# Kernel tuning notes

Hardware: AMD Instinct MI355X
Metric: run time of the kernel (lower is better)

## Reference

```python
import jax, jax.numpy as jnp
import numpy as np

B, S, D = 2, 2048, 2048
NH, NKV, HD = 16, 4, 128
REP = NH // NKV
EPS = 1e-6
ROPE_THETA = 1e6


def setup_inputs() -> dict:
    key = jax.random.key(0)
    ks = jax.random.split(key, 6)
    x = jax.random.normal(ks[0], (B, S, D), jnp.float32)
    # real rotary embeddings: [S, HD]
    inv_freq = 1.0 / (ROPE_THETA ** (np.arange(0, HD, 2, dtype=np.float64) / HD))
    freqs = np.outer(np.arange(S, dtype=np.float64), inv_freq)
    emb = np.concatenate([freqs, freqs], axis=-1)
    cos = jnp.asarray(np.cos(emb), jnp.float32)
    sin = jnp.asarray(np.sin(emb), jnp.float32)
    scale = 1.0 / np.sqrt(D)
    Wq = jax.random.normal(ks[1], (D, NH * HD), jnp.float32) * scale   # [in, out]
    Wk = jax.random.normal(ks[2], (D, NKV * HD), jnp.float32) * scale
    Wv = jax.random.normal(ks[3], (D, NKV * HD), jnp.float32) * scale
    Wo = jax.random.normal(ks[4], (NH * HD, D), jnp.float32) * (1.0 / np.sqrt(NH * HD))
    q_norm_w = jnp.ones((HD,), jnp.float32)
    k_norm_w = jnp.ones((HD,), jnp.float32)
    return dict(x=x, cos=cos, sin=sin, Wq=Wq, Wk=Wk, Wv=Wv, Wo=Wo,
                q_norm_w=q_norm_w, k_norm_w=k_norm_w)


def _rms_norm(h, w):
    var = jnp.mean(h * h, axis=-1, keepdims=True)
    return w * (h * jax.lax.rsqrt(var + EPS))


def _rotate_half(h):
    h1, h2 = jnp.split(h, 2, axis=-1)
    return jnp.concatenate([-h2, h1], axis=-1)


def reference(x, cos, sin, Wq, Wk, Wv, Wo, q_norm_w, k_norm_w):
    b, s, _ = x.shape
    q = (x @ Wq).reshape(b, s, NH, HD)
    k = (x @ Wk).reshape(b, s, NKV, HD)
    v = (x @ Wv).reshape(b, s, NKV, HD)
    # per-head QK RMSNorm
    q = _rms_norm(q, q_norm_w)
    k = _rms_norm(k, k_norm_w)
    # RoPE: cos/sin [S,HD] -> broadcast over batch and heads
    c = cos[None, :, None, :]
    s_ = sin[None, :, None, :]
    q = q * c + _rotate_half(q) * s_
    k = k * c + _rotate_half(k) * s_
    # GQA: group q heads per kv head instead of materializing repeat_kv
    qg = q.reshape(b, s, NKV, REP, HD)
    scores = jnp.einsum('bqgrd,bkgd->bgrqk', qg, k) / np.sqrt(HD)
    causal = jnp.tril(jnp.ones((s, s), bool))  # [q,k]
    scores = jnp.where(causal, scores, -jnp.inf)
    probs = jax.nn.softmax(scores.astype(jnp.float32), axis=-1).astype(q.dtype)
    out = jnp.einsum('bgrqk,bkgd->bqgrd', probs, v).reshape(b, s, NH * HD)
    return out @ Wo
```

## Files before the change

### kernel.cpp

```cpp
#include <hip/hip_runtime.h>
#include <hip/hip_bf16.h>
#include <math.h>

#define B_ 2
#define S_ 2048
#define D_ 2048
#define NH_ 16
#define NKV_ 4
#define HD_ 128
#define EPS_ 1e-6f
#define SCALE_ 0.08838834764831845f
#define LOG2E_ 1.4426950408889634f
#define NQKV_ 3072
#define KOFF_ 2048
#define VOFF_ 2560

typedef float f32x4 __attribute__((ext_vector_type(4)));
typedef short bf16x8 __attribute__((ext_vector_type(8)));
typedef short short4v __attribute__((ext_vector_type(4)));
typedef float float4v __attribute__((ext_vector_type(4)));
typedef unsigned uint2v __attribute__((ext_vector_type(2)));

static __device__ __forceinline__ short f2bf(float f) {
    union { float f; unsigned u; } x{f};
    unsigned r = (x.u + 0x7fff + ((x.u >> 16) & 1)) >> 16;
    return (short)r;
}
static __device__ __forceinline__ float bf2f(short s) {
    union { unsigned u; float f; } x; x.u = ((unsigned)(unsigned short)s) << 16; return x.f;
}
static __device__ __forceinline__ unsigned pack_bf2(float a, float b) {
    return __builtin_amdgcn_perm(__builtin_bit_cast(unsigned, b),
                                 __builtin_bit_cast(unsigned, a), 0x07060302u);
}

#define AS1(p) ((const __attribute__((address_space(1))) void*)(p))
#define AS3(p) ((__attribute__((address_space(3))) void*)(p))
static __device__ __forceinline__ void async16(const void* g, void* l) {
    __builtin_amdgcn_global_load_lds(AS1(g), AS3(l), 16, 0, 0);
}

__global__ __launch_bounds__(256) void cast_kernel(const float* __restrict__ in,
                                                   short* __restrict__ out) {
    size_t i = ((size_t)blockIdx.x * 256 + threadIdx.x) * 4;
    float4v v = *(const float4v*)(in + i);
    short4v o; o.x = f2bf(v.x); o.y = f2bf(v.y); o.z = f2bf(v.z); o.w = f2bf(v.w);
    *(short4v*)(out + i) = o;
}

__global__ __launch_bounds__(256) void transpose_cast_kernel(const float* __restrict__ in,
                                                             short* __restrict__ out,
                                                             int K, int N) {
    __shared__ float tile[64][65];
    const int n0 = blockIdx.x * 64, k0 = blockIdx.y * 64;
    const int tid = threadIdx.x;
    for (int r = 0; r < 16; ++r) {
        int k = r * 4 + (tid >> 6);
        int n = tid & 63;
        tile[k][n] = in[(size_t)(k0 + k) * N + n0 + n];
    }
    __syncthreads();
    for (int r = 0; r < 4; ++r) {
        int n  = r * 16 + (tid >> 4);
        int kk = (tid & 15) * 4;
        short4v o4;
        o4.x = f2bf(tile[kk + 0][n]); o4.y = f2bf(tile[kk + 1][n]);
        o4.z = f2bf(tile[kk + 2][n]); o4.w = f2bf(tile[kk + 3][n]);
        *(short4v*)&out[(size_t)(n0 + n) * K + k0 + kk] = o4;
    }
}

template<typename TC>
__global__ __launch_bounds__(256) void gemm_tt_kernel(const short* __restrict__ A,
                                                      const short* __restrict__ Bt,
                                                      TC* __restrict__ C,
                                                      int M, int N, int K) {
    __shared__ short As[128 * 32];
    __shared__ short Bs[128 * 32];

    const int tid  = threadIdx.x;
    const int bn   = blockIdx.x, bm = blockIdx.y;
    const int wave = tid >> 6, lane = tid & 63;
    const int quad = lane >> 4, l16 = lane & 15;
    const int wr = wave >> 1, wc = wave & 1;

    f32x4 acc[4][4];
    for (int i = 0; i < 4; ++i)
        for (int j = 0; j < 4; ++j) acc[i][j] = (f32x4){0.f, 0.f, 0.f, 0.f};

    const short* Abase = A  + (size_t)(bm * 128) * K;
    const short* Bbase = Bt + (size_t)(bn * 128) * K;

    int ci0 = wave * 128 + lane;
    for (int k0 = 0; k0 < K; k0 += 32) {
        __syncthreads();
        for (int t = 0; t < 2; ++t) {
            int ci = ci0 + t * 64;
            int r  = ci >> 2;
            int c  = ((ci & 3) - (r >> 1)) & 3;
            size_t goff = (size_t)r * K + k0 + c * 8;
            async16(Abase + goff, &As[ci * 8]);
            async16(Bbase + goff, &Bs[ci * 8]);
        }
        __syncthreads();

        bf16x8 af[4], bfv[4];
        for (int mt = 0; mt < 4; ++mt) {
            int r = wr * 64 + mt * 16 + l16;
            af[mt] = *(const bf16x8*)&As[r * 32 + (((quad + (r >> 1)) & 3) * 8)];
        }
        for (int nt = 0; nt < 4; ++nt) {
            int r = wc * 64 + nt * 16 + l16;
            bfv[nt] = *(const bf16x8*)&Bs[r * 32 + (((quad + (r >> 1)) & 3) * 8)];
        }
        for (int mt = 0; mt < 4; ++mt)
            for (int nt = 0; nt < 4; ++nt)
                acc[mt][nt] = __builtin_amdgcn_mfma_f32_16x16x32_bf16(
                    af[mt], bfv[nt], acc[mt][nt], 0, 0, 0);
    }

    for (int mt = 0; mt < 4; ++mt)
        for (int nt = 0; nt < 4; ++nt)
            for (int j = 0; j < 4; ++j) {
                int row = bm * 128 + wr * 64 + mt * 16 + quad * 4 + j;
                int col = bn * 128 + wc * 64 + nt * 16 + l16;
                float v = acc[mt][nt][j];
                if constexpr (__is_same(TC, short))
                    C[(size_t)row * N + col] = f2bf(v);
                else
                    C[(size_t)row * N + col] = v;
            }
}

template<int NHEADS, bool HEAD_MAJOR>
__global__ __launch_bounds__(256) void rope_rms_kernel(const short* __restrict__ qkv,
                                                       int coloff,
                                                       const float* __restrict__ cosb,
                                                       const float* __restrict__ sinb,
                                                       const float* __restrict__ w,
                                                       short* __restrict__ out,
                                                       float outscale) {
    const int r    = blockIdx.x * 4 + (threadIdx.x >> 6);
    const int lane = threadIdx.x & 63;
    const int tok  = r / NHEADS, head = r % NHEADS;
    const int spos = tok & (S_ - 1);
    const short* row = qkv + (size_t)tok * NQKV_ + coloff + head * HD_;
    float h1 = bf2f(row[lane]), h2 = bf2f(row[lane + 64]);
    float ss = h1 * h1 + h2 * h2;
    for (int off = 1; off < 64; off <<= 1) ss += __shfl_xor(ss, off);
    float rstd = rsqrtf(ss * (1.0f / HD_) + EPS_);
    float n1 = h1 * rstd * w[lane];
    float n2 = h2 * rstd * w[lane + 64];
    float c  = cosb[spos * HD_ + lane];
    float sn = sinb[spos * HD_ + lane];
    size_t o;
    if (HEAD_MAJOR) {
        int b = tok >> 11, s = tok & (S_ - 1);
        o = ((size_t)(b * NHEADS + head) * S_ + s) * HD_;
    } else {
        o = ((size_t)tok * NHEADS + head) * HD_;
    }
    out[o + lane]      = f2bf((n1 * c - n2 * sn) * outscale);
    out[o + lane + 64] = f2bf((n2 * c + n1 * sn) * outscale);
}

__global__ __launch_bounds__(256) void vtrans_kernel(const short* __restrict__ qkv,
                                                     short* __restrict__ vt) {
    __shared__ short tile[64][71];
    const int s0 = blockIdx.x * 64, d0 = blockIdx.y * 64;
    const int g = blockIdx.z & 3, b = blockIdx.z >> 2;
    const int tid = threadIdx.x;
    for (int r = 0; r < 16; ++r) {
        int s = r * 4 + (tid >> 6);
        int d = tid & 63;
        tile[s][d] = qkv[(size_t)(b * S_ + s0 + s) * NQKV_ + VOFF_ + g * HD_ + d0 + d];
    }
    __syncthreads();
    for (int r = 0; r < 16; ++r) {
        int d = r * 4 + (tid >> 6);
        int s = tid & 63;
        vt[((size_t)(b * NKV_ + g) * HD_ + d0 + d) * S_ + s0 + s] = tile[s][d];
    }
}

__global__ __launch_bounds__(256, 2) void attn_kernel(const short* __restrict__ qr,
                                                      const short* __restrict__ kg,
                                                      const short* __restrict__ vt,
                                                      short* __restrict__ aout) {
    __shared__ short Ks[2][64 * 128];
    __shared__ short Vs[2][128 * 64];

    const int lin = blockIdx.x;
    const int b  = lin & 1;
    const int g  = (lin >> 1) & 3;
    const int hq = (lin >> 3) & 3;
    const int pr = lin >> 5;
    const int h  = g * 4 + hq;

    const int wave = threadIdx.x >> 6, lane = threadIdx.x & 63;
    const int quad = lane >> 4, l16 = lane & 15;

    const short* kbase = kg + (size_t)(b * NKV_ + g) * S_ * HD_;
    const short* vbase = vt + (size_t)(b * NKV_ + g) * HD_ * S_;

    for (int pass = 0; pass < 2; ++pass) {
        const int qt    = pass ? (31 - pr) : pr;
        const int iters = qt + 1;
        const int qrow  = qt * 64 + wave * 16 + l16;

        bf16x8 qf[4];
        {
            const short* qp = qr + ((size_t)(b * S_ + qrow) * NH_ + h) * HD_;
            for (int ks = 0; ks < 4; ++ks)
                qf[ks] = *(const bf16x8*)(qp + ks * 32 + quad * 8);
        }

        f32x4 o[8];
        for (int i = 0; i < 8; ++i) o[i] = (f32x4){0.f, 0.f, 0.f, 0.f};
        float m_i = -INFINITY, l_i = 0.f;

        auto stage = [&](int kt, int bsel) {
            const short* kt_base = kbase + (size_t)kt * 64 * HD_;
            const short* vt_base = vbase + kt * 64;
            for (int t = 0; t < 4; ++t) {
                int ci  = (wave * 4 + t) * 64 + lane;
                int key = ci >> 4;
                int c   = (ci & 15) ^ ((key ^ (key >> 2)) & 15);
                async16(kt_base + key * HD_ + c * 8, &Ks[bsel][ci * 8]);
            }
            for (int t = 0; t < 4; ++t) {
                int ci = (wave * 4 + t) * 64 + lane;
                int d  = ci >> 3;
                int c  = (ci & 7) ^ (d & 7);
                async16(vt_base + (size_t)d * S_ + c * 8, &Vs[bsel][ci * 8]);
            }
        };

        stage(0, 0);
        int buf = 0;
        for (int kt = 0; kt < iters; ++kt) {
            __syncthreads();
            if (kt + 1 < iters) stage(kt + 1, buf ^ 1);

            f32x4 acc[4];
            for (int t = 0; t < 4; ++t) acc[t] = (f32x4){0.f, 0.f, 0.f, 0.f};
            for (int t = 0; t < 4; ++t) {
                int lk = ((t >> 1) << 5) + ((l16 >> 2) << 3) + ((t & 1) << 2) + (l16 & 3);
                const short* kp = &Ks[buf][lk * 128];
                int pm = (lk ^ (lk >> 2)) & 15;
                for (int ks = 0; ks < 4; ++ks) {
                    bf16x8 kf = *(const bf16x8*)(kp + (((ks * 4 + quad) ^ pm) * 8));
                    acc[t] = __builtin_amdgcn_mfma_f32_16x16x32_bf16(kf, qf[ks], acc[t], 0, 0, 0);
                }
            }
            const int key_base = kt * 64;
            if (key_base + 63 > qt * 64 + wave * 16) {
                for (int t = 0; t < 4; ++t)
                    for (int j = 0; j < 4; ++j) {
                        int kl = key_base + ((t >> 1) << 5) + (quad << 3) + ((t & 1) << 2) + j;
                        if (kl > qrow) acc[t][j] = -INFINITY;
                    }
            }
            float mx = m_i;
            for (int t = 0; t < 4; ++t)
                for (int j = 0; j < 4; ++j) mx = fmaxf(mx, acc[t][j]);
            mx = fmaxf(mx, __shfl_xor(mx, 16));
            mx = fmaxf(mx, __shfl_xor(mx, 32));
            float al = __builtin_amdgcn_exp2f(m_i - mx);
            m_i = mx;
            float rs = 0.f;
            float p[4][4];
            for (int t = 0; t < 4; ++t)
                for (int j = 0; j < 4; ++j) {
                    float e = __builtin_amdgcn_exp2f(acc[t][j] - mx);
                    p[t][j] = e;
                    rs += e;
                }
            rs += __shfl_xor(rs, 16);
            rs += __shfl_xor(rs, 32);
            l_i = al * l_i + rs;
            for (int d8 = 0; d8 < 8; ++d8)
                for (int j = 0; j < 4; ++j) o[d8][j] *= al;
            unsigned pk[2][4];
            for (int grp = 0; grp < 2; ++grp) {
                pk[grp][0] = pack_bf2(p[2 * grp][0],     p[2 * grp][1]);
                pk[grp][1] = pack_bf2(p[2 * grp][2],     p[2 * grp][3]);
                pk[grp][2] = pack_bf2(p[2 * grp + 1][0], p[2 * grp + 1][1]);
                pk[grp][3] = pack_bf2(p[2 * grp + 1][2], p[2 * grp + 1][3]);
            }
            for (int grp = 0; grp < 2; ++grp) {
                union { unsigned u[4]; bf16x8 v; } pb;
                for (int i = 0; i < 4; ++i) pb.u[i] = pk[grp][i];
                for (int d8 = 0; d8 < 8; ++d8) {
                    int d = d8 * 16 + l16;
                    bf16x8 vf = *(const bf16x8*)&Vs[buf][d * 64 + (((grp * 4 + quad) ^ (d & 7)) * 8)];
                    o[d8] = __builtin_amdgcn_mfma_f32_16x16x32_bf16(vf, pb.v, o[d8], 0, 0, 0);
                }
            }
            buf ^= 1;
        }
        float il = 1.0f / l_i;
        short* op = aout + ((size_t)(b * S_ + qrow) * NH_ + h) * HD_ + quad * 4;
        for (int d8 = 0; d8 < 8; ++d8) {
            uint2v wv;
            wv.x = ((unsigned)(unsigned short)f2bf(o[d8][0] * il)) |
                   ((unsigned)(unsigned short)f2bf(o[d8][1] * il) << 16);
            wv.y = ((unsigned)(unsigned short)f2bf(o[d8][2] * il)) |
                   ((unsigned)(unsigned short)f2bf(o[d8][3] * il) << 16);
            *(uint2v*)(op + d8 * 16) = wv;
        }
        __syncthreads();
    }
}

extern "C" void kernel_launch(void* const* d_in, const int* in_sizes, int n_in,
                              void* d_out, int out_size, void* d_ws, size_t ws_size,
                              hipStream_t stream) {
    (void)in_sizes; (void)n_in; (void)out_size; (void)ws_size;
    const float* x    = (const float*)d_in[0];
    const float* cosb = (const float*)d_in[1];
    const float* sinb = (const float*)d_in[2];
    const float* Wq   = (const float*)d_in[3];
    const float* Wk   = (const float*)d_in[4];
    const float* Wv   = (const float*)d_in[5];
    const float* Wo   = (const float*)d_in[6];
    const float* qw   = (const float*)d_in[7];
    const float* kw   = (const float*)d_in[8];
    float* out = (float*)d_out;

    char* ws = (char*)d_ws;
    short* qkv    = (short*)ws;  ws += (size_t)4096 * NQKV_ * 2;
    short* xb     = (short*)ws;  ws += (size_t)4096 * 2048 * 2;
    short* Wt     = (short*)ws;  ws += (size_t)NQKV_ * 2048 * 2;
    short* Wot    = (short*)ws;  ws += (size_t)2048 * 2048 * 2;
    short* q_rope = (short*)ws;  ws += (size_t)4096 * 2048 * 2;
    short* k_rope = (short*)ws;  ws += (size_t)4096 * 512 * 2;
    short* vt     = (short*)ws;  ws += (size_t)4096 * 512 * 2;
    short* a_out  = (short*)ws;  ws += (size_t)4096 * 2048 * 2;

    const int M = B_ * S_;

    cast_kernel<<<M * 2048 / 1024, 256, 0, stream>>>(x, xb);
    transpose_cast_kernel<<<dim3(2048 / 64, 2048 / 64), 256, 0, stream>>>(Wq, Wt, 2048, 2048);
    transpose_cast_kernel<<<dim3(512 / 64, 2048 / 64), 256, 0, stream>>>(Wk, Wt + (size_t)KOFF_ * 2048, 2048, 512);
    transpose_cast_kernel<<<dim3(512 / 64, 2048 / 64), 256, 0, stream>>>(Wv, Wt + (size_t)VOFF_ * 2048, 2048, 512);
    transpose_cast_kernel<<<dim3(2048 / 64, 2048 / 64), 256, 0, stream>>>(Wo, Wot, 2048, 2048);

    gemm_tt_kernel<short><<<dim3(NQKV_ / 128, M / 128), 256, 0, stream>>>(
        xb, Wt, qkv, M, NQKV_, 2048);

    rope_rms_kernel<NH_, false><<<M * NH_ / 4, 256, 0, stream>>>(
        qkv, 0, cosb, sinb, qw, q_rope, SCALE_ * LOG2E_);
    rope_rms_kernel<NKV_, true><<<M * NKV_ / 4, 256, 0, stream>>>(
        qkv, KOFF_, cosb, sinb, kw, k_rope, 1.0f);
    vtrans_kernel<<<dim3(S_ / 64, HD_ / 64, B_ * NKV_), 256, 0, stream>>>(qkv, vt);

    attn_kernel<<<512, 256, 0, stream>>>(q_rope, k_rope, vt, a_out);

    gemm_tt_kernel<float><<<dim3(D_ / 128, M / 128), 256, 0, stream>>>(
        a_out, Wot, out, M, D_, 2048);
}
```

Baseline: 330.3 us.

## Fuse QKV GEMM with RMSNorm, RoPE and V transpose; merge weight transposes

Merges the four weight transpose-cast launches into one kernel that picks its source by block index. Folds per-head RMSNorm, RoPE and the V transpose into the epilogue of the QKV projection GEMM. This removes the intermediate qkv buffer round trip and three extra launches. The epilogue stages the tile through shared memory with a cross-wave sum-of-squares reduction, which adds epilogue cost and LDS pressure to the GEMM.

Measured after the change: 329.6 us. About the same (-0.2%).

```diff
diff --git a/kernel.cpp b/kernel.cpp
--- a/kernel.cpp
+++ b/kernel.cpp
@@ -11,7 +11,6 @@
 #define EPS_ 1e-6f
 #define SCALE_ 0.08838834764831845f
 #define LOG2E_ 1.4426950408889634f
-#define NQKV_ 3072
 #define KOFF_ 2048
 #define VOFF_ 2560
 
@@ -48,16 +47,25 @@
     *(short4v*)(out + i) = o;
 }
 
-__global__ __launch_bounds__(256) void transpose_cast_kernel(const float* __restrict__ in,
-                                                             short* __restrict__ out,
-                                                             int K, int N) {
+__global__ __launch_bounds__(256) void transpose_all_kernel(const float* __restrict__ Wq,
+                                                            const float* __restrict__ Wk,
+                                                            const float* __restrict__ Wv,
+                                                            const float* __restrict__ Wo,
+                                                            short* __restrict__ Wt,
+                                                            short* __restrict__ Wot) {
     __shared__ float tile[64][65];
-    const int n0 = blockIdx.x * 64, k0 = blockIdx.y * 64;
+    const int bx = blockIdx.x, by = blockIdx.y;
+    const float* src; short* dst; int N, nb;
+    if (bx < 32)      { src = Wq; dst = Wt;                         N = 2048; nb = bx; }
+    else if (bx < 40) { src = Wk; dst = Wt + (size_t)KOFF_ * 2048;  N = 512;  nb = bx - 32; }
+    else if (bx < 48) { src = Wv; dst = Wt + (size_t)VOFF_ * 2048;  N = 512;  nb = bx - 40; }
+    else              { src = Wo; dst = Wot;                        N = 2048; nb = bx - 48; }
+    const int n0 = nb * 64, k0 = by * 64;
     const int tid = threadIdx.x;
     for (int r = 0; r < 16; ++r) {
         int k = r * 4 + (tid >> 6);
         int n = tid & 63;
-        tile[k][n] = in[(size_t)(k0 + k) * N + n0 + n];
+        tile[k][n] = src[(size_t)(k0 + k) * N + n0 + n];
     }
     __syncthreads();
     for (int r = 0; r < 4; ++r) {
@@ -66,7 +74,7 @@
         short4v o4;
         o4.x = f2bf(tile[kk + 0][n]); o4.y = f2bf(tile[kk + 1][n]);
         o4.z = f2bf(tile[kk + 2][n]); o4.w = f2bf(tile[kk + 3][n]);
-        *(short4v*)&out[(size_t)(n0 + n) * K + k0 + kk] = o4;
+        *(short4v*)&dst[(size_t)(n0 + n) * 2048 + k0 + kk] = o4;
     }
 }
 
@@ -132,54 +140,137 @@
             }
 }
 
-template<int NHEADS, bool HEAD_MAJOR>
-__global__ __launch_bounds__(256) void rope_rms_kernel(const short* __restrict__ qkv,
-                                                       int coloff,
-                                                       const float* __restrict__ cosb,
-                                                       const float* __restrict__ sinb,
-                                                       const float* __restrict__ w,
-                                                       short* __restrict__ out,
-                                                       float outscale) {
-    const int r    = blockIdx.x * 4 + (threadIdx.x >> 6);
-    const int lane = threadIdx.x & 63;
-    const int tok  = r / NHEADS, head = r % NHEADS;
-    const int spos = tok & (S_ - 1);
-    const short* row = qkv + (size_t)tok * NQKV_ + coloff + head * HD_;
-    float h1 = bf2f(row[lane]), h2 = bf2f(row[lane + 64]);
-    float ss = h1 * h1 + h2 * h2;
-    for (int off = 1; off < 64; off <<= 1) ss += __shfl_xor(ss, off);
-    float rstd = rsqrtf(ss * (1.0f / HD_) + EPS_);
-    float n1 = h1 * rstd * w[lane];
-    float n2 = h2 * rstd * w[lane + 64];
-    float c  = cosb[spos * HD_ + lane];
-    float sn = sinb[spos * HD_ + lane];
-    size_t o;
-    if (HEAD_MAJOR) {
-        int b = tok >> 11, s = tok & (S_ - 1);
-        o = ((size_t)(b * NHEADS + head) * S_ + s) * HD_;
-    } else {
-        o = ((size_t)tok * NHEADS + head) * HD_;
-    }
-    out[o + lane]      = f2bf((n1 * c - n2 * sn) * outscale);
-    out[o + lane + 64] = f2bf((n2 * c + n1 * sn) * outscale);
-}
-
-__global__ __launch_bounds__(256) void vtrans_kernel(const short* __restrict__ qkv,
-                                                     short* __restrict__ vt) {
-    __shared__ short tile[64][71];
-    const int s0 = blockIdx.x * 64, d0 = blockIdx.y * 64;
-    const int g = blockIdx.z & 3, b = blockIdx.z >> 2;
-    const int tid = threadIdx.x;
-    for (int r = 0; r < 16; ++r) {
-        int s = r * 4 + (tid >> 6);
-        int d = tid & 63;
-        tile[s][d] = qkv[(size_t)(b * S_ + s0 + s) * NQKV_ + VOFF_ + g * HD_ + d0 + d];
-    }
+__global__ __launch_bounds__(256) void qkv_fused_kernel(const short* __restrict__ xb,
+                                                        const short* __restrict__ Wt,
+                                                        const float* __restrict__ cosb,
+                                                        const float* __restrict__ sinb,
+                                                        const float* __restrict__ qw,
+                                                        const float* __restrict__ kw,
+                                                        short* __restrict__ q_rope,
+                                                        short* __restrict__ k_rope,
+                                                        short* __restrict__ vtr) {
+    __shared__ short tile[128 * 128];
+    __shared__ float ss2[2][128];
+    short* As = tile;
+    short* Bs = tile + 4096;
+
+    const int tid  = threadIdx.x;
+    const int bn   = blockIdx.x, bm = blockIdx.y;
+    const int wave = tid >> 6, lane = tid & 63;
+    const int quad = lane >> 4, l16 = lane & 15;
+    const int wr = wave >> 1, wc = wave & 1;
+
+    f32x4 acc[4][4];
+    for (int i = 0; i < 4; ++i)
+        for (int j = 0; j < 4; ++j) acc[i][j] = (f32x4){0.f, 0.f, 0.f, 0.f};
+
+    const short* Abase = xb + (size_t)(bm * 128) * 2048;
+    const short* Bbase = Wt + (size_t)(bn * 128) * 2048;
+
+    int ci0 = wave * 128 + lane;
+    for (int k0 = 0; k0 < 2048; k0 += 32) {
+        __syncthreads();
+        for (int t = 0; t < 2; ++t) {
+            int ci = ci0 + t * 64;
+            int r  = ci >> 2;
+            int c  = ((ci & 3) - (r >> 1)) & 3;
+            size_t goff = (size_t)r * 2048 + k0 + c * 8;
+            async16(Abase + goff, &As[ci * 8]);
+            async16(Bbase + goff, &Bs[ci * 8]);
+        }
+        __syncthreads();
+
+        bf16x8 af[4], bfv[4];
+        for (int mt = 0; mt < 4; ++mt) {
+            int r = wr * 64 + mt * 16 + l16;
+            af[mt] = *(const bf16x8*)&As[r * 32 + (((quad + (r >> 1)) & 3) * 8)];
+        }
+        for (int nt = 0; nt < 4; ++nt) {
+            int r = wc * 64 + nt * 16 + l16;
+            bfv[nt] = *(const bf16x8*)&Bs[r * 32 + (((quad + (r >> 1)) & 3) * 8)];
+        }
+        for (int mt = 0; mt < 4; ++mt)
+            for (int nt = 0; nt < 4; ++nt)
+                acc[mt][nt] = __builtin_amdgcn_mfma_f32_16x16x32_bf16(
+                    af[mt], bfv[nt], acc[mt][nt], 0, 0, 0);
+    }
+
+    if (bn >= 20) {
+        const int g = bn - 20;
+        for (int mt = 0; mt < 4; ++mt) {
+            int tok0 = bm * 128 + wr * 64 + mt * 16 + quad * 4;
+            int bb = tok0 >> 11, s0 = tok0 & (S_ - 1);
+            for (int nt = 0; nt < 4; ++nt) {
+                int d = wc * 64 + nt * 16 + l16;
+                short4v o4;
+                o4.x = f2bf(acc[mt][nt][0]); o4.y = f2bf(acc[mt][nt][1]);
+                o4.z = f2bf(acc[mt][nt][2]); o4.w = f2bf(acc[mt][nt][3]);
+                *(short4v*)&vtr[((size_t)(bb * NKV_ + g) * HD_ + d) * S_ + s0] = o4;
+            }
+        }
+        return;
+    }
+
     __syncthreads();
-    for (int r = 0; r < 16; ++r) {
-        int d = r * 4 + (tid >> 6);
-        int s = tid & 63;
-        vt[((size_t)(b * NKV_ + g) * HD_ + d0 + d) * S_ + s0 + s] = tile[s][d];
+    {
+        float pss[4][4];
+        for (int mt = 0; mt < 4; ++mt)
+            for (int j = 0; j < 4; ++j) {
+                float s = 0.f;
+                for (int nt = 0; nt < 4; ++nt) s += acc[mt][nt][j] * acc[mt][nt][j];
+                pss[mt][j] = s;
+            }
+        for (int off = 1; off < 16; off <<= 1)
+            for (int mt = 0; mt < 4; ++mt)
+                for (int j = 0; j < 4; ++j)
+                    pss[mt][j] += __shfl_xor(pss[mt][j], off);
+        if (l16 == 0)
+            for (int mt = 0; mt < 4; ++mt)
+                for (int j = 0; j < 4; ++j)
+                    ss2[wc][wr * 64 + mt * 16 + quad * 4 + j] = pss[mt][j];
+    }
+    for (int mt = 0; mt < 4; ++mt)
+        for (int nt = 0; nt < 4; ++nt)
+            for (int j = 0; j < 4; ++j)
+                tile[(wr * 64 + mt * 16 + quad * 4 + j) * 128 + wc * 64 + nt * 16 + l16]
+                    = f2bf(acc[mt][nt][j]);
+    __syncthreads();
+
+    const bool isQ = (bn < 16);
+    const float osc = isQ ? (SCALE_ * LOG2E_) : 1.0f;
+    const float* w = isQ ? qw : kw;
+    for (int it = 0; it < 8; ++it) {
+        int idx = tid + it * 256;
+        int row = idx >> 4, seg = idx & 15;
+        int tok = bm * 128 + row;
+        int bb = tok >> 11, s = tok & (S_ - 1);
+        float rstd = rsqrtf((ss2[0][row] + ss2[1][row]) * (1.0f / HD_) + EPS_);
+        int c0 = seg * 8, p0 = (seg ^ 8) * 8;
+        bf16x8 ta = *(const bf16x8*)&tile[row * 128 + c0];
+        bf16x8 tb = *(const bf16x8*)&tile[row * 128 + p0];
+        float sgn = (seg < 8) ? -1.0f : 1.0f;
+        unsigned ov[4];
+        for (int i2 = 0; i2 < 4; ++i2) {
+            float r0, r1;
+            for (int k = 0; k < 2; ++k) {
+                int i = i2 * 2 + k;
+                float n1 = bf2f(ta[i]) * rstd * w[c0 + i];
+                float n2 = bf2f(tb[i]) * rstd * w[p0 + i];
+                float cs = cosb[(size_t)s * HD_ + c0 + i];
+                float sn = sinb[(size_t)s * HD_ + c0 + i];
+                float o = (n1 * cs + sgn * n2 * sn) * osc;
+                if (k == 0) r0 = o; else r1 = o;
+            }
+            ov[i2] = ((unsigned)(unsigned short)f2bf(r0)) |
+                     ((unsigned)(unsigned short)f2bf(r1) << 16);
+        }
+        short* dst = isQ
+            ? q_rope + ((size_t)(bb * S_ + s) * NH_ + bn) * HD_ + c0
+            : k_rope + ((size_t)(bb * NKV_ + (bn - 16)) * S_ + s) * HD_ + c0;
+        uint2v w0; w0.x = ov[0]; w0.y = ov[1];
+        uint2v w1; w1.x = ov[2]; w1.y = ov[3];
+        *(uint2v*)dst = w0;
+        *(uint2v*)(dst + 4) = w1;
     }
 }
 
@@ -329,9 +420,8 @@
     float* out = (float*)d_out;
 
     char* ws = (char*)d_ws;
-    short* qkv    = (short*)ws;  ws += (size_t)4096 * NQKV_ * 2;
     short* xb     = (short*)ws;  ws += (size_t)4096 * 2048 * 2;
-    short* Wt     = (short*)ws;  ws += (size_t)NQKV_ * 2048 * 2;
+    short* Wt     = (short*)ws;  ws += (size_t)3072 * 2048 * 2;
     short* Wot    = (short*)ws;  ws += (size_t)2048 * 2048 * 2;
     short* q_rope = (short*)ws;  ws += (size_t)4096 * 2048 * 2;
     short* k_rope = (short*)ws;  ws += (size_t)4096 * 512 * 2;
@@ -341,19 +431,10 @@
     const int M = B_ * S_;
 
     cast_kernel<<<M * 2048 / 1024, 256, 0, stream>>>(x, xb);
-    transpose_cast_kernel<<<dim3(2048 / 64, 2048 / 64), 256, 0, stream>>>(Wq, Wt, 2048, 2048);
-    transpose_cast_kernel<<<dim3(512 / 64, 2048 / 64), 256, 0, stream>>>(Wk, Wt + (size_t)KOFF_ * 2048, 2048, 512);
-    transpose_cast_kernel<<<dim3(512 / 64, 2048 / 64), 256, 0, stream>>>(Wv, Wt + (size_t)VOFF_ * 2048, 2048, 512);
-    transpose_cast_kernel<<<dim3(2048 / 64, 2048 / 64), 256, 0, stream>>>(Wo, Wot, 2048, 2048);
-
-    gemm_tt_kernel<short><<<dim3(NQKV_ / 128, M / 128), 256, 0, stream>>>(
-        xb, Wt, qkv, M, NQKV_, 2048);
-
-    rope_rms_kernel<NH_, false><<<M * NH_ / 4, 256, 0, stream>>>(
-        qkv, 0, cosb, sinb, qw, q_rope, SCALE_ * LOG2E_);
-    rope_rms_kernel<NKV_, true><<<M * NKV_ / 4, 256, 0, stream>>>(
-        qkv, KOFF_, cosb, sinb, kw, k_rope, 1.0f);
-    vtrans_kernel<<<dim3(S_ / 64, HD_ / 64, B_ * NKV_), 256, 0, stream>>>(qkv, vt);
+    transpose_all_kernel<<<dim3(80, 32), 256, 0, stream>>>(Wq, Wk, Wv, Wo, Wt, Wot);
+
+    qkv_fused_kernel<<<dim3(24, M / 128), 256, 0, stream>>>(
+        xb, Wt, cosb, sinb, qw, kw, q_rope, k_rope, vt);
 
     attn_kernel<<<512, 256, 0, stream>>>(q_rope, k_rope, vt, a_out);
 
```
